# Optimization experiments

Hardware: AMD Instinct MI355X
Metric: run time of the kernel (lower is better)

## Reference

```python
import math
import jax, jax.numpy as jnp
import numpy as np

B, T, D, H = 2, 2048, 768, 12
Dh = D // H


def setup_inputs() -> dict:
    key = jax.random.key(0)
    ks = jax.random.split(key, 4)
    s = 1.0 / math.sqrt(D)
    x = jax.random.normal(ks[0], (B, T, D), dtype=jnp.float32)
    Wq = jax.random.normal(ks[1], (D, D), dtype=jnp.float32) * s
    Wk = jax.random.normal(ks[2], (D, D), dtype=jnp.float32) * s
    Wv = jax.random.normal(ks[3], (D, D), dtype=jnp.float32) * s
    bq = jnp.zeros((D,), dtype=jnp.float32)
    bk = jnp.zeros((D,), dtype=jnp.float32)
    bv = jnp.zeros((D,), dtype=jnp.float32)
    # additive causal mask, broadcastable to [B,H,T,T]
    causal = jnp.triu(jnp.ones((T, T), dtype=bool), k=1)
    attn_mask = jnp.where(causal, jnp.float32(-1e9), jnp.float32(0.0))[None, None]
    return {"x": x, "Wq": Wq, "bq": bq, "Wk": Wk, "bk": bk,
            "Wv": Wv, "bv": bv, "attn_mask": attn_mask}


def reference(x, Wq, bq, Wk, bk, Wv, bv, attn_mask):
    # torch Linear: y = x @ W.T + b
    q = (jnp.einsum('btd,ed->bte', x, Wq) + bq).reshape(B, T, H, Dh).transpose(0, 2, 1, 3)
    k = (jnp.einsum('btd,ed->bte', x, Wk) + bk).reshape(B, T, H, Dh).transpose(0, 2, 1, 3)
    v = (jnp.einsum('btd,ed->bte', x, Wv) + bv).reshape(B, T, H, Dh).transpose(0, 2, 1, 3)
    scores = jnp.einsum('bhqd,bhkd->bhqk', q, k) / jnp.float32(math.sqrt(Dh))
    scores = scores + attn_mask
    attn = jax.nn.softmax(scores, axis=-1)  # [B,H,T,T]
    heads = jnp.einsum('bhqk,bhkd->bhqd', attn, v)
    heads_out = heads.transpose(0, 2, 1, 3)  # [B,T,H,Dh]
    return heads_out, attn
```

## Files before the change

kernel.cpp:

```cpp
#include <hip/hip_runtime.h>

typedef float f32x16 __attribute__((ext_vector_type(16)));
typedef float f32x4  __attribute__((ext_vector_type(4)));
typedef short s16x8  __attribute__((ext_vector_type(8)));
typedef short s16x4  __attribute__((ext_vector_type(4)));

constexpr int Bn = 2, Tn = 2048, Dn = 768, Hn = 12, DHn = 64;
constexpr int NX = Bn * Tn * Dn;
constexpr int NW = Dn * Dn;
constexpr float SC2f = 0.125f * 1.44269504088896f;

__device__ __forceinline__ unsigned short f2bf(float f) {
    union { float f; unsigned int i; } c; c.f = f;
    unsigned int u = c.i;
    u += 0x7fffu + ((u >> 16) & 1u);
    return (unsigned short)(u >> 16);
}
__device__ __forceinline__ unsigned int cvtpk(float lo, float hi) {
    unsigned int r;
    asm("v_cvt_pk_bf16_f32 %0, %1, %2" : "=v"(r) : "v"(lo), "v"(hi));
    return r;
}
__device__ __forceinline__ s16x8 ld_cvt(const float* p) {
    f32x4 a = *(const f32x4*)p;
    f32x4 b = *(const f32x4*)(p + 4);
    union { unsigned int u[4]; s16x8 v; } r;
    r.u[0] = cvtpk(a[0], a[1]); r.u[1] = cvtpk(a[2], a[3]);
    r.u[2] = cvtpk(b[0], b[1]); r.u[3] = cvtpk(b[2], b[3]);
    return r.v;
}
__device__ __forceinline__ void barrier_lgkm() {
    asm volatile("s_waitcnt lgkmcnt(0)" ::: "memory");
    __builtin_amdgcn_s_barrier();
    asm volatile("" ::: "memory");
}

__global__ __launch_bounds__(256) void proj_staged(
    const float* __restrict__ x,
    const float* __restrict__ wq, const float* __restrict__ wk,
    const float* __restrict__ wv,
    const float* __restrict__ bq, const float* __restrict__ bk,
    const float* __restrict__ bv,
    unsigned short* __restrict__ qo, unsigned short* __restrict__ kfo,
    unsigned short* __restrict__ vfo)
{
    __shared__ unsigned short lA[2][128 * 40];
    __shared__ unsigned short lB[2][128 * 40];

    const int z = blockIdx.z;
    const bool vt = (z == 2);
    const float* W = (z == 0) ? wq : (z == 1) ? wk : wv;
    const float* bias = (z == 0) ? bq : (z == 1) ? bk : bv;
    const int tid = threadIdx.x, lane = tid & 63, wid = tid >> 6;
    const int lq = lane & 31, g = lane >> 5;
    const int mb = vt ? blockIdx.y : blockIdx.x;
    const int nb = vt ? blockIdx.x : blockIdx.y;
    const float* Am = vt ? W : x;
    const float* Bm = vt ? x : W;

    const int srow = tid >> 2, sch = tid & 3;
    const float* ag0 = Am + (size_t)(mb * 128 +      srow) * Dn + sch * 8;
    const float* ag1 = Am + (size_t)(mb * 128 + 64 + srow) * Dn + sch * 8;
    const float* bg0 = Bm + (size_t)(nb * 128 +      srow) * Dn + sch * 8;
    const float* bg1 = Bm + (size_t)(nb * 128 + 64 + srow) * Dn + sch * 8;
    const int sd0 = srow * 40 + sch * 8;
    const int sd1 = (64 + srow) * 40 + sch * 8;

    f32x16 acc[2][2];
#pragma unroll
    for (int am = 0; am < 2; ++am)
#pragma unroll
        for (int bn = 0; bn < 2; ++bn)
#pragma unroll
            for (int i = 0; i < 16; ++i) acc[am][bn][i] = 0.f;

    {
        s16x8 a0 = ld_cvt(ag0), a1 = ld_cvt(ag1);
        s16x8 b0 = ld_cvt(bg0), b1 = ld_cvt(bg1);
        *(s16x8*)&lA[0][sd0] = a0; *(s16x8*)&lA[0][sd1] = a1;
        *(s16x8*)&lB[0][sd0] = b0; *(s16x8*)&lB[0][sd1] = b1;
    }
    const int ar = (wid & 1) * 64 + lq;
    const int br = (wid >> 1) * 64 + lq;

    for (int kt = 0; kt < 24; ++kt) {
        const int cur = kt & 1;
        s16x8 a0, a1, b0, b1;
        if (kt < 23) {
            a0 = ld_cvt(ag0 + (kt + 1) * 32);
            a1 = ld_cvt(ag1 + (kt + 1) * 32);
            b0 = ld_cvt(bg0 + (kt + 1) * 32);
            b1 = ld_cvt(bg1 + (kt + 1) * 32);
        }
        barrier_lgkm();
        s16x8 afr[2][2], bfr[2][2];
#pragma unroll
        for (int am = 0; am < 2; ++am)
#pragma unroll
            for (int kc = 0; kc < 2; ++kc)
                afr[am][kc] = *(const s16x8*)&lA[cur][(ar + am * 32) * 40 + (2 * kc + g) * 8];
#pragma unroll
        for (int bn = 0; bn < 2; ++bn)
#pragma unroll
            for (int kc = 0; kc < 2; ++kc)
                bfr[bn][kc] = *(const s16x8*)&lB[cur][(br + bn * 32) * 40 + (2 * kc + g) * 8];
#pragma unroll
        for (int kc = 0; kc < 2; ++kc)
#pragma unroll
            for (int am = 0; am < 2; ++am)
#pragma unroll
                for (int bn = 0; bn < 2; ++bn)
                    acc[am][bn] = __builtin_amdgcn_mfma_f32_32x32x16_bf16(
                        afr[am][kc], bfr[bn][kc], acc[am][bn], 0, 0, 0);
        if (kt < 23) {
            *(s16x8*)&lA[cur ^ 1][sd0] = a0; *(s16x8*)&lA[cur ^ 1][sd1] = a1;
            *(s16x8*)&lB[cur ^ 1][sd0] = b0; *(s16x8*)&lB[cur ^ 1][sd1] = b1;
        }
    }

    if (z == 0) {
#pragma unroll
        for (int bn = 0; bn < 2; ++bn) {
            const int e = nb * 128 + (wid >> 1) * 64 + bn * 32 + lq;
            const float bvl = bias[e];
            const int h = e >> 6, dh = e & 63;
#pragma unroll
            for (int am = 0; am < 2; ++am)
#pragma unroll
                for (int r = 0; r < 16; ++r) {
                    const int t = mb * 128 + (wid & 1) * 64 + am * 32 + ((r & 3) + 8 * (r >> 2) + 4 * g);
                    const int b = t >> 11, tl = t & (Tn - 1);
                    qo[((size_t)(b * Hn + h) * Tn + tl) * DHn + dh] = f2bf((acc[am][bn][r] + bvl) * SC2f);
                }
        }
    } else if (z == 1) {
#pragma unroll
        for (int bn = 0; bn < 2; ++bn) {
            const int e = nb * 128 + (wid >> 1) * 64 + bn * 32 + lq;
            const float bvl = bias[e];
            const int h = e >> 6, dh = e & 63;
            const int cK = dh >> 4, gK = (dh >> 3) & 1, el = dh & 7;
#pragma unroll
            for (int am = 0; am < 2; ++am)
#pragma unroll
                for (int r = 0; r < 16; ++r) {
                    const int t = mb * 128 + (wid & 1) * 64 + am * 32 + ((r & 3) + 8 * (r >> 2) + 4 * g);
                    const int b = t >> 11, tl = t & (Tn - 1);
                    const int kt2 = tl >> 5, lrow = tl & 31;
                    kfo[(((size_t)(b * Hn + h) * 64 + kt2) * 4 + cK) * 512
                        + (lrow + 32 * gK) * 8 + el] = f2bf(acc[am][bn][r] + bvl);
                }
        }
    } else {
#pragma unroll
        for (int am = 0; am < 2; ++am)
#pragma unroll
            for (int r = 0; r < 16; ++r) {
                const int e = mb * 128 + (wid & 1) * 64 + am * 32 + ((r & 3) + 8 * (r >> 2) + 4 * g);
                const float bvl = bias[e];
                const int h = e >> 6, dhp = e & 63;
                const int o = dhp >> 5, lqv = dhp & 31;
#pragma unroll
                for (int bn = 0; bn < 2; ++bn) {
                    const int t = nb * 128 + (wid >> 1) * 64 + bn * 32 + lq;
                    const int b = t >> 11, tl = t & (Tn - 1);
                    const int kt2 = tl >> 5, kcol = tl & 31;
                    const int c2 = kcol >> 4, rem = kcol & 15;
                    const int gV = (rem >> 2) & 1;
                    const int j = (rem & 3) + ((rem >> 3) << 2);
                    vfo[((((size_t)(b * Hn + h) * 64 + kt2) * 2 + c2) * 2 + o) * 512
                        + (lqv + 32 * gV) * 8 + j] = f2bf(acc[am][bn][r] + bvl);
                }
            }
    }
}

__global__ __launch_bounds__(256) void attn_main(
    const unsigned short* __restrict__ Q,
    const unsigned short* __restrict__ Kf,
    const unsigned short* __restrict__ Vf,
    float* __restrict__ heads,
    float* __restrict__ attn)
{
    __shared__ float P[32 * 256];
    __shared__ float pls[4][32];

    const int tid = threadIdx.x, lane = tid & 63, wid = tid >> 6;
    const int lq = lane & 31, g = lane >> 5;
    const int n2 = ((int)blockIdx.x & 7) * 192 + ((int)blockIdx.x >> 3);
    const int bh = n2 >> 6;
    const int s  = 63 - (n2 & 63);
    const int qbase = s * 32;

    const unsigned short* Qb = Q  + ((size_t)bh * Tn + qbase) * DHn;
    const unsigned short* Kb = Kf + (size_t)bh * 131072 + lane * 8;
    const unsigned short* Vb = Vf + (size_t)bh * 131072 + lane * 8;
    const int swz = (lq & 7) << 2;

    s16x8 qf[4];
#pragma unroll
    for (int c = 0; c < 4; ++c)
        qf[c] = *(const s16x8*)(Qb + lq * DHn + c * 16 + g * 8);

    float ls = 0.f;
    for (int kt = wid; kt <= s; kt += 4) {
        const unsigned short* kb = Kb + (size_t)kt * 2048;
        f32x16 acc;
#pragma unroll
        for (int i = 0; i < 16; ++i) acc[i] = 0.f;
#pragma unroll
        for (int c = 0; c < 4; ++c)
            acc = __builtin_amdgcn_mfma_f32_32x32x16_bf16(
                *(const s16x8*)(kb + c * 512), qf[c], acc, 0, 0, 0);
        if (kt == s) {
#pragma unroll
            for (int r = 0; r < 16; ++r) {
                const int koff = (r & 3) + 8 * (r >> 2) + 4 * g;
                ls += (koff <= lq) ? exp2f(acc[r]) : 0.f;
            }
        } else {
#pragma unroll
            for (int r = 0; r < 16; ++r) ls += exp2f(acc[r]);
        }
    }
    ls += __shfl_xor(ls, 32);
    if (g == 0) pls[wid][lq] = ls;
    __syncthreads();
    const float rl = 1.f / (pls[0][lq] + pls[1][lq] + pls[2][lq] + pls[3][lq]);

    f32x16 o0, o1;
#pragma unroll
    for (int i = 0; i < 16; ++i) { o0[i] = 0.f; o1[i] = 0.f; }

    for (int p = 0; p < 8; ++p) {
#pragma unroll
        for (int j = 0; j < 2; ++j) {
            const int kt = p * 8 + wid + 4 * j;
            const int slot = (kt & 7) * 32;
            if (kt <= s) {
                const unsigned short* kb = Kb + (size_t)kt * 2048;
                f32x16 acc;
#pragma unroll
                for (int i = 0; i < 16; ++i) acc[i] = 0.f;
#pragma unroll
                for (int c = 0; c < 4; ++c)
                    acc = __builtin_amdgcn_mfma_f32_32x32x16_bf16(
                        *(const s16x8*)(kb + c * 512), qf[c], acc, 0, 0, 0);
                const bool diag = (kt == s);
                float pv[16];
#pragma unroll
                for (int r = 0; r < 16; ++r) {
                    const int koff = (r & 3) + 8 * (r >> 2) + 4 * g;
                    float e = exp2f(acc[r]) * rl;
                    pv[r] = (diag && koff > lq) ? 0.f : e;
                }
#pragma unroll
                for (int a = 0; a < 4; ++a) {
                    f32x4 w;
                    w[0]=pv[4*a+0]; w[1]=pv[4*a+1]; w[2]=pv[4*a+2]; w[3]=pv[4*a+3];
                    *(f32x4*)&P[lq * 256 + slot + ((4 * g + 8 * a) ^ swz)] = w;
                }
                union { unsigned int uu[4]; s16x8 v; } P0, P1;
                P0.uu[0]=cvtpk(pv[0],pv[1]);   P0.uu[1]=cvtpk(pv[2],pv[3]);
                P0.uu[2]=cvtpk(pv[4],pv[5]);   P0.uu[3]=cvtpk(pv[6],pv[7]);
                P1.uu[0]=cvtpk(pv[8],pv[9]);   P1.uu[1]=cvtpk(pv[10],pv[11]);
                P1.uu[2]=cvtpk(pv[12],pv[13]); P1.uu[3]=cvtpk(pv[14],pv[15]);
                const unsigned short* vb = Vb + (size_t)kt * 2048;
#pragma unroll
                for (int c2 = 0; c2 < 2; ++c2) {
                    const s16x8 pa = c2 ? P1.v : P0.v;
                    o0 = __builtin_amdgcn_mfma_f32_32x32x16_bf16(
                        pa, *(const s16x8*)(vb + (c2 * 2 + 0) * 512), o0, 0, 0, 0);
                    o1 = __builtin_amdgcn_mfma_f32_32x32x16_bf16(
                        pa, *(const s16x8*)(vb + (c2 * 2 + 1) * 512), o1, 0, 0, 0);
                }
            } else if (kt < 8 || kt - 8 <= s) {
                f32x4 z; z[0]=0.f; z[1]=0.f; z[2]=0.f; z[3]=0.f;
#pragma unroll
                for (int a = 0; a < 4; ++a)
                    *(f32x4*)&P[lq * 256 + slot + ((4 * g + 8 * a) ^ swz)] = z;
            }
        }
        barrier_lgkm();
#pragma unroll
        for (int j2 = 0; j2 < 8; ++j2) {
            const int row = wid * 8 + j2;
            f32x4 w = *(const f32x4*)&P[row * 256 + ((lane * 4) ^ ((row & 7) << 2))];
            __builtin_nontemporal_store(w,
                (f32x4*)(attn + ((size_t)bh * Tn + qbase + row) * Tn + p * 256 + lane * 4));
        }
        barrier_lgkm();
    }

    if (wid) {
#pragma unroll
        for (int r = 0; r < 16; ++r) {
            const int tr = (r & 3) + 8 * (r >> 2) + 4 * g;
            P[(wid - 1) * 2048 + tr * 64 + lq]      = o0[r];
            P[(wid - 1) * 2048 + tr * 64 + 32 + lq] = o1[r];
        }
    }
    __syncthreads();
    if (!wid) {
        const int b = bh / Hn, hh = bh % Hn;
#pragma unroll
        for (int r = 0; r < 16; ++r) {
            const int tr = (r & 3) + 8 * (r >> 2) + 4 * g;
            float* base = heads + ((size_t)(b * Tn + (qbase + tr))) * Dn + hh * DHn;
            base[lq]      = o0[r] + P[tr * 64 + lq]
                          + P[2048 + tr * 64 + lq] + P[4096 + tr * 64 + lq];
            base[32 + lq] = o1[r] + P[tr * 64 + 32 + lq]
                          + P[2048 + tr * 64 + 32 + lq] + P[4096 + tr * 64 + 32 + lq];
        }
    }
}

extern "C" void kernel_launch(void* const* d_in, const int* in_sizes, int n_in,
                              void* d_out, int out_size, void* d_ws, size_t ws_size,
                              hipStream_t stream) {
    (void)in_sizes; (void)n_in; (void)out_size; (void)ws_size;
    const float* x  = (const float*)d_in[0];
    const float* Wq = (const float*)d_in[1];
    const float* bq = (const float*)d_in[2];
    const float* Wk = (const float*)d_in[3];
    const float* bk = (const float*)d_in[4];
    const float* Wv = (const float*)d_in[5];
    const float* bv = (const float*)d_in[6];

    float* heads = (float*)d_out;
    float* attn  = heads + (size_t)Bn * Tn * Dn;

    unsigned short* qws  = (unsigned short*)d_ws;
    unsigned short* kws  = qws + NX;
    unsigned short* vtws = kws + NX;

    proj_staged<<<dim3(32, 6, 3), 256, 0, stream>>>(x, Wq, Wk, Wv, bq, bk, bv,
                                                    qws, kws, vtws);
    attn_main<<<1536, 256, 0, stream>>>(qws, kws, vtws, heads, attn);
}
```

Baseline: 131.1 us.

## Double-buffer attention probability staging to drop one barrier per iteration

The probability staging tile is split into two 128-column halves that alternate between iterations. Each iteration now covers four key tiles (one per wave) instead of eight, and only one barrier per iteration is kept instead of two, so compute of the next tile can overlap with the global store of the previous one. The cost is twice as many loop iterations, each storing narrower 128-column row segments. It also relies on the alternating buffers to avoid write-after-read hazards without the second barrier.

```diff
diff --git a/kernel.cpp b/kernel.cpp
--- a/kernel.cpp
+++ b/kernel.cpp
@@ -182,7 +182,7 @@
     float* __restrict__ heads,
     float* __restrict__ attn)
 {
-    __shared__ float P[32 * 256];
+    __shared__ float P2[8192];
     __shared__ float pls[4][32];
 
     const int tid = threadIdx.x, lane = tid & 63, wid = tid >> 6;
@@ -232,72 +232,70 @@
 #pragma unroll
     for (int i = 0; i < 16; ++i) { o0[i] = 0.f; o1[i] = 0.f; }
 
-    for (int p = 0; p < 8; ++p) {
-#pragma unroll
-        for (int j = 0; j < 2; ++j) {
-            const int kt = p * 8 + wid + 4 * j;
-            const int slot = (kt & 7) * 32;
-            if (kt <= s) {
-                const unsigned short* kb = Kb + (size_t)kt * 2048;
-                f32x16 acc;
-#pragma unroll
-                for (int i = 0; i < 16; ++i) acc[i] = 0.f;
-#pragma unroll
-                for (int c = 0; c < 4; ++c)
-                    acc = __builtin_amdgcn_mfma_f32_32x32x16_bf16(
-                        *(const s16x8*)(kb + c * 512), qf[c], acc, 0, 0, 0);
-                const bool diag = (kt == s);
-                float pv[16];
-#pragma unroll
-                for (int r = 0; r < 16; ++r) {
-                    const int koff = (r & 3) + 8 * (r >> 2) + 4 * g;
-                    float e = exp2f(acc[r]) * rl;
-                    pv[r] = (diag && koff > lq) ? 0.f : e;
-                }
-#pragma unroll
-                for (int a = 0; a < 4; ++a) {
-                    f32x4 w;
-                    w[0]=pv[4*a+0]; w[1]=pv[4*a+1]; w[2]=pv[4*a+2]; w[3]=pv[4*a+3];
-                    *(f32x4*)&P[lq * 256 + slot + ((4 * g + 8 * a) ^ swz)] = w;
-                }
-                union { unsigned int uu[4]; s16x8 v; } P0, P1;
-                P0.uu[0]=cvtpk(pv[0],pv[1]);   P0.uu[1]=cvtpk(pv[2],pv[3]);
-                P0.uu[2]=cvtpk(pv[4],pv[5]);   P0.uu[3]=cvtpk(pv[6],pv[7]);
-                P1.uu[0]=cvtpk(pv[8],pv[9]);   P1.uu[1]=cvtpk(pv[10],pv[11]);
-                P1.uu[2]=cvtpk(pv[12],pv[13]); P1.uu[3]=cvtpk(pv[14],pv[15]);
-                const unsigned short* vb = Vb + (size_t)kt * 2048;
-#pragma unroll
-                for (int c2 = 0; c2 < 2; ++c2) {
-                    const s16x8 pa = c2 ? P1.v : P0.v;
-                    o0 = __builtin_amdgcn_mfma_f32_32x32x16_bf16(
-                        pa, *(const s16x8*)(vb + (c2 * 2 + 0) * 512), o0, 0, 0, 0);
-                    o1 = __builtin_amdgcn_mfma_f32_32x32x16_bf16(
-                        pa, *(const s16x8*)(vb + (c2 * 2 + 1) * 512), o1, 0, 0, 0);
-                }
-            } else if (kt < 8 || kt - 8 <= s) {
-                f32x4 z; z[0]=0.f; z[1]=0.f; z[2]=0.f; z[3]=0.f;
-#pragma unroll
-                for (int a = 0; a < 4; ++a)
-                    *(f32x4*)&P[lq * 256 + slot + ((4 * g + 8 * a) ^ swz)] = z;
-            }
+    for (int p = 0; p < 16; ++p) {
+        float* buf = P2 + (p & 1) * 4096;
+        const int kt = p * 4 + wid;
+        if (kt <= s) {
+            const unsigned short* kb = Kb + (size_t)kt * 2048;
+            f32x16 acc;
+#pragma unroll
+            for (int i = 0; i < 16; ++i) acc[i] = 0.f;
+#pragma unroll
+            for (int c = 0; c < 4; ++c)
+                acc = __builtin_amdgcn_mfma_f32_32x32x16_bf16(
+                    *(const s16x8*)(kb + c * 512), qf[c], acc, 0, 0, 0);
+            const bool diag = (kt == s);
+            float pv[16];
+#pragma unroll
+            for (int r = 0; r < 16; ++r) {
+                const int koff = (r & 3) + 8 * (r >> 2) + 4 * g;
+                float e = exp2f(acc[r]) * rl;
+                pv[r] = (diag && koff > lq) ? 0.f : e;
+            }
+#pragma unroll
+            for (int a = 0; a < 4; ++a) {
+                f32x4 w;
+                w[0]=pv[4*a+0]; w[1]=pv[4*a+1]; w[2]=pv[4*a+2]; w[3]=pv[4*a+3];
+                *(f32x4*)&buf[lq * 128 + wid * 32 + ((4 * g + 8 * a) ^ swz)] = w;
+            }
+            union { unsigned int uu[4]; s16x8 v; } P0, P1;
+            P0.uu[0]=cvtpk(pv[0],pv[1]);   P0.uu[1]=cvtpk(pv[2],pv[3]);
+            P0.uu[2]=cvtpk(pv[4],pv[5]);   P0.uu[3]=cvtpk(pv[6],pv[7]);
+            P1.uu[0]=cvtpk(pv[8],pv[9]);   P1.uu[1]=cvtpk(pv[10],pv[11]);
+            P1.uu[2]=cvtpk(pv[12],pv[13]); P1.uu[3]=cvtpk(pv[14],pv[15]);
+            const unsigned short* vb = Vb + (size_t)kt * 2048;
+#pragma unroll
+            for (int c2 = 0; c2 < 2; ++c2) {
+                const s16x8 pa = c2 ? P1.v : P0.v;
+                o0 = __builtin_amdgcn_mfma_f32_32x32x16_bf16(
+                    pa, *(const s16x8*)(vb + (c2 * 2 + 0) * 512), o0, 0, 0, 0);
+                o1 = __builtin_amdgcn_mfma_f32_32x32x16_bf16(
+                    pa, *(const s16x8*)(vb + (c2 * 2 + 1) * 512), o1, 0, 0, 0);
+            }
+        } else if (kt < 8 || kt - 8 <= s) {
+            f32x4 z; z[0]=0.f; z[1]=0.f; z[2]=0.f; z[3]=0.f;
+#pragma unroll
+            for (int a = 0; a < 4; ++a)
+                *(f32x4*)&buf[lq * 128 + wid * 32 + ((4 * g + 8 * a) ^ swz)] = z;
         }
         barrier_lgkm();
 #pragma unroll
-        for (int j2 = 0; j2 < 8; ++j2) {
-            const int row = wid * 8 + j2;
-            f32x4 w = *(const f32x4*)&P[row * 256 + ((lane * 4) ^ ((row & 7) << 2))];
+        for (int j2 = 0; j2 < 4; ++j2) {
+            const int row = wid * 8 + j2 * 2 + (lane >> 5);
+            const int c   = (lane & 31) * 4;
+            f32x4 w = *(const f32x4*)&buf[row * 128 + (c ^ ((row & 7) << 2))];
             __builtin_nontemporal_store(w,
-                (f32x4*)(attn + ((size_t)bh * Tn + qbase + row) * Tn + p * 256 + lane * 4));
-        }
-        barrier_lgkm();
-    }
+                (f32x4*)(attn + ((size_t)bh * Tn + qbase + row) * Tn + p * 128 + c));
+        }
+    }
+    barrier_lgkm();
 
     if (wid) {
 #pragma unroll
         for (int r = 0; r < 16; ++r) {
             const int tr = (r & 3) + 8 * (r >> 2) + 4 * g;
-            P[(wid - 1) * 2048 + tr * 64 + lq]      = o0[r];
-            P[(wid - 1) * 2048 + tr * 64 + 32 + lq] = o1[r];
+            P2[(wid - 1) * 2048 + tr * 64 + lq]      = o0[r];
+            P2[(wid - 1) * 2048 + tr * 64 + 32 + lq] = o1[r];
         }
     }
     __syncthreads();
@@ -307,10 +305,10 @@
         for (int r = 0; r < 16; ++r) {
             const int tr = (r & 3) + 8 * (r >> 2) + 4 * g;
             float* base = heads + ((size_t)(b * Tn + (qbase + tr))) * Dn + hh * DHn;
-            base[lq]      = o0[r] + P[tr * 64 + lq]
-                          + P[2048 + tr * 64 + lq] + P[4096 + tr * 64 + lq];
-            base[32 + lq] = o1[r] + P[tr * 64 + 32 + lq]
-                          + P[2048 + tr * 64 + 32 + lq] + P[4096 + tr * 64 + 32 + lq];
+            base[lq]      = o0[r] + P2[tr * 64 + lq]
+                          + P2[2048 + tr * 64 + lq] + P2[4096 + tr * 64 + lq];
+            base[32 + lq] = o1[r] + P2[tr * 64 + 32 + lq]
+                          + P2[2048 + tr * 64 + 32 + lq] + P2[4096 + tr * 64 + 32 + lq];
         }
     }
 }
```

Result: no change. 131.2 us (+0.1%).
